# Optimization experiments

Hardware: AMD Instinct MI355X
Metric: run time of the kernel (lower is better)

The kernel has to match this reference:

```python
import jax, jax.numpy as jnp
import numpy as np

B, Q, K, D, H, DH = 4, 512, 4096, 1024, 8, 128  # qk_channels=v_channels=out=1024

def setup_inputs() -> dict:
    key = jax.random.key(0)
    ks = jax.random.split(key, 5)
    s = 1.0 / np.sqrt(D)
    return {
        "inputs_q": jax.random.normal(ks[0], (B, Q, D), jnp.float32),
        "inputs_kv": jax.random.normal(ks[1], (B, K, D), jnp.float32),
        "Wq": jax.random.normal(ks[2], (D, H, DH), jnp.float32) * s,
        "Wkv": jax.random.normal(ks[3], (D, H, 2 * DH), jnp.float32) * s,
        "Wproj": jax.random.normal(ks[4], (H, DH, D), jnp.float32) * (1.0 / np.sqrt(H * DH)),
        "b_proj": jnp.zeros((D,), jnp.float32),
    }

def reference(inputs_q, inputs_kv, Wq, Wkv, Wproj, b_proj):
    # QKV projections (no bias)
    q = jnp.einsum('bqd,dhe->bqhe', inputs_q, Wq)          # [B,Q,H,DH]
    kv = jnp.einsum('bkd,dhe->bkhe', inputs_kv, Wkv)        # [B,K,H,2*DH]
    k, v = kv[..., :DH], kv[..., DH:]
    # scaled dot-product attention (softmax in fp32, per source)
    attn = jnp.einsum('bqhd,bkhd->bhqk', q, k) / np.sqrt(DH)
    attn = jax.nn.softmax(attn.astype(jnp.float32), axis=-1).astype(v.dtype)
    o = jnp.einsum('bhqk,bkhd->bqhd', attn, v)              # [B,Q,H,DH]
    # output projection contracting (head, head_dim), with bias
    return jnp.einsum('bqhd,hdo->bqo', o, Wproj) + b_proj   # [B,Q,D]
```

## Files before the change

### kernel.cpp

```cpp
#include <hip/hip_runtime.h>
#include <hip/hip_bf16.h>
#include <cstdint>

typedef unsigned short u16;
typedef unsigned int u32;
typedef __bf16 bf16x8 __attribute__((ext_vector_type(8)));
typedef u16 u16x8 __attribute__((ext_vector_type(8)));
typedef u16 u16x4 __attribute__((ext_vector_type(4)));
typedef float f32x4 __attribute__((ext_vector_type(4)));

#define MFMA16(a, b, c) __builtin_amdgcn_mfma_f32_16x16x32_bf16(a, b, c, 0, 0, 0)

__device__ __forceinline__ void async16(const void* g, void* s) {
    __builtin_amdgcn_global_load_lds((const __attribute__((address_space(1))) void*)g,
                                     (__attribute__((address_space(3))) void*)s, 16, 0, 0);
}

__device__ __forceinline__ u16 f2bf(float f) {
    u32 u; __builtin_memcpy(&u, &f, 4);
    u = u + 0x7fffu + ((u >> 16) & 1u);
    return (u16)(u >> 16);
}

__global__ __launch_bounds__(256) void convert_inputs(const float* __restrict__ inq,
                                                      u16* __restrict__ Aq,
                                                      const float* __restrict__ inkv,
                                                      u16* __restrict__ Akv) {
    const int blk = blockIdx.x;
    const float* in; u16* out; size_t i;
    if (blk < 1024) { in = inq;  out = Aq;  i = (size_t)blk * 256 + threadIdx.x; }
    else            { in = inkv; out = Akv; i = (size_t)(blk - 1024) * 256 + threadIdx.x; }
    const float4* p = (const float4*)in + i * 2;
    const float4 a = p[0], b = p[1];
    u16x8 v;
    v[0] = f2bf(a.x); v[1] = f2bf(a.y); v[2] = f2bf(a.z); v[3] = f2bf(a.w);
    v[4] = f2bf(b.x); v[5] = f2bf(b.y); v[6] = f2bf(b.z); v[7] = f2bf(b.w);
    ((u16x8*)out)[i] = v;
}

__global__ __launch_bounds__(256) void prep_weights(const float* __restrict__ Wq,  u16* __restrict__ WqT,
                                                    const float* __restrict__ Wkv, u16* __restrict__ WkvT,
                                                    const float* __restrict__ Wp,  u16* __restrict__ WpT) {
    __shared__ u16 t[64][65];
    const int blk = blockIdx.x;
    const float* in; u16* out; int R, C, bx, by;
    if (blk < 256)      { in = Wq;  out = WqT;  R = 1024; C = 1024; bx = blk & 15;  by = blk >> 4; }
    else if (blk < 768) { in = Wkv; out = WkvT; R = 1024; C = 2048; bx = (blk - 256) & 31; by = (blk - 256) >> 5; }
    else                { in = Wp;  out = WpT;  R = 1024; C = 1024; bx = (blk - 768) & 15; by = (blk - 768) >> 4; }
    const int r0 = by << 6, c0 = bx << 6;
    const int tid = threadIdx.x;
#pragma unroll
    for (int i = 0; i < 16; i++) {
        int idx = i * 256 + tid;
        int r = idx >> 6, c = idx & 63;
        t[r][c] = f2bf(in[(size_t)(r0 + r) * C + c0 + c]);
    }
    __syncthreads();
#pragma unroll
    for (int i = 0; i < 16; i++) {
        int idx = i * 256 + tid;
        int c = idx >> 6, r = idx & 63;
        out[(size_t)(c0 + c) * R + r0 + r] = t[r][c];
    }
}

template <bool OUTF32, int NT>
__global__ __launch_bounds__(256) void gemm_bt(const u16* __restrict__ A,
                                               const u16* __restrict__ B,
                                               void* __restrict__ Cv,
                                               const float* __restrict__ bias,
                                               int M, int N, int K) {
    constexpr int NJ = NT / 32;
    __shared__ __align__(16) u16 As[128 * 64];
    __shared__ __align__(16) u16 Bs[NT * 64];
    const int tid = threadIdx.x;
    const int wave = tid >> 6, lane = tid & 63;
    const int lrow = lane & 15, quad = lane >> 4;
    const int nb = N / NT;
    const int bx = blockIdx.x % nb, by = blockIdx.x / nb;
    const long m0 = (long)by << 7, n0 = (long)bx * NT;
    const int wm = (wave >> 1) << 6, wn = (wave & 1) * (NT / 2);

    const f32x4 fz = {0.f, 0.f, 0.f, 0.f};
    f32x4 acc[4][NJ];
#pragma unroll
    for (int i = 0; i < 4; i++)
#pragma unroll
        for (int j = 0; j < NJ; j++) acc[i][j] = fz;

    const int srow = wave * 8 + (lane >> 3);
    const int scol = ((lane & 7) ^ (lane >> 3)) << 3;
    const u16* Ag = A + (m0 + srow) * K + scol;
    const u16* Bg = B + (n0 + srow) * K + scol;
    u16* AsW = &As[wave * 512];
    u16* BsW = &Bs[wave * 512];

    for (int k0 = 0; k0 < K; k0 += 64) {
        __syncthreads();
#pragma unroll
        for (int c = 0; c < 4; c++)
            async16(Ag + (long)c * 32 * K + k0, AsW + c * 2048);
#pragma unroll
        for (int c = 0; c < NT / 32; c++)
            async16(Bg + (long)c * 32 * K + k0, BsW + c * 2048);
        __syncthreads();
#pragma unroll
        for (int c = 0; c < 2; c++) {
            bf16x8 af[4], bfr[NJ];
#pragma unroll
            for (int i = 0; i < 4; i++) {
                const int row = wm + i * 16 + lrow;
                af[i] = *(const bf16x8*)&As[row * 64 + (((c * 4 + quad) ^ (row & 7)) << 3)];
            }
#pragma unroll
            for (int j = 0; j < NJ; j++) {
                const int row = wn + j * 16 + lrow;
                bfr[j] = *(const bf16x8*)&Bs[row * 64 + (((c * 4 + quad) ^ (row & 7)) << 3)];
            }
#pragma unroll
            for (int i = 0; i < 4; i++)
#pragma unroll
                for (int j = 0; j < NJ; j++)
                    acc[i][j] = MFMA16(bfr[j], af[i], acc[i][j]);
        }
    }
#pragma unroll
    for (int i = 0; i < 4; i++) {
        const long row = m0 + wm + i * 16 + lrow;
#pragma unroll
        for (int j = 0; j < NJ; j++) {
            const long colb = n0 + wn + j * 16 + quad * 4;
            if (OUTF32) {
                f32x4 v = acc[i][j];
                if (bias) v += *(const f32x4*)&bias[colb];
                *(f32x4*)&((float*)Cv)[row * N + colb] = v;
            } else {
                u16x4 pk;
#pragma unroll
                for (int r = 0; r < 4; r++) pk[r] = f2bf(acc[i][j][r]);
                *(u16x4*)&((u16*)Cv)[row * N + colb] = pk;
            }
        }
    }
}

__global__ __launch_bounds__(512, 2) void gemm_kv256(const u16* __restrict__ A,
                                                     const u16* __restrict__ B,
                                                     u16* __restrict__ C,
                                                     u16* __restrict__ Vt) {
    constexpr int K = 1024, N = 2048, NT = 16;
    __shared__ __align__(16) u16 As[2][256 * 64];
    __shared__ __align__(16) u16 Bs[2][256 * 64];
    const int tid = threadIdx.x;
    const int wave = tid >> 6, lane = tid & 63;
    const int lrow = lane & 15, quad = lane >> 4;
    const int wMi = wave >> 2, wNi = wave & 3;
    const int wm = wMi * 128, wn = wNi * 64;
    const int wg = blockIdx.x;
    const int swz = (wg & 7) * 64 + (wg >> 3);
    const int bx = swz & 7, by = swz >> 3;
    const long m0 = (long)by << 8, n0 = (long)bx << 8;

    const int srow = tid >> 3;
    const int scol = ((tid & 7) ^ (srow & 7)) << 3;
    const u16* Ag = A + (m0 + srow) * K + scol;
    const u16* Bg = B + (n0 + srow) * K + scol;
    const int sdst = tid * 8;

    auto stgA = [&](int bi, int h, int kt) {
        async16(Ag + (size_t)(h * 128) * K + kt * 64,      &As[bi][h * 8192 + sdst]);
        async16(Ag + (size_t)(h * 128 + 64) * K + kt * 64, &As[bi][h * 8192 + 4096 + sdst]);
    };
    auto stgB = [&](int bi, int h, int kt) {
        async16(Bg + (size_t)(h * 128) * K + kt * 64,      &Bs[bi][h * 8192 + sdst]);
        async16(Bg + (size_t)(h * 128 + 64) * K + kt * 64, &Bs[bi][h * 8192 + 4096 + sdst]);
    };

    stgB(0, 0, 0); stgB(0, 1, 0); stgA(0, 0, 0); stgA(0, 1, 0);
    stgB(1, 0, 1); stgB(1, 1, 1); stgA(1, 0, 1);

    const f32x4 fz = {0.f, 0.f, 0.f, 0.f};
    f32x4 acc[8][4];
#pragma unroll
    for (int i = 0; i < 8; i++)
#pragma unroll
        for (int j = 0; j < 4; j++) acc[i][j] = fz;

    asm volatile("s_waitcnt vmcnt(6)" ::: "memory");
    __builtin_amdgcn_s_barrier();

    bf16x8 av[4][2], bv[4][2];
    for (int t = 0; t < NT; ++t) {
        const int cur = t & 1, nxt = cur ^ 1;
#pragma unroll
        for (int i = 0; i < 4; i++) {
            const int row = wm + i * 16 + lrow;
#pragma unroll
            for (int c = 0; c < 2; c++)
                av[i][c] = *(const bf16x8*)&As[cur][row * 64 + (((c * 4 + quad) ^ (row & 7)) << 3)];
        }
#pragma unroll
        for (int j = 0; j < 4; j++) {
            const int row = wn + j * 16 + lrow;
#pragma unroll
            for (int c = 0; c < 2; c++)
                bv[j][c] = *(const bf16x8*)&Bs[cur][row * 64 + (((c * 4 + quad) ^ (row & 7)) << 3)];
        }
        if (t + 1 < NT) stgA(nxt, 1, t + 1);
        __builtin_amdgcn_s_barrier();
        asm volatile("s_waitcnt lgkmcnt(0)" ::: "memory");
        __builtin_amdgcn_sched_barrier(0);
        __builtin_amdgcn_s_setprio(1);
#pragma unroll
        for (int i = 0; i < 4; i++)
#pragma unroll
            for (int j = 0; j < 2; j++)
#pragma unroll
                for (int c = 0; c < 2; c++)
                    acc[i][j] = MFMA16(av[i][c], bv[j][c], acc[i][j]);
        __builtin_amdgcn_s_setprio(0);
        __builtin_amdgcn_s_barrier();
        if (t + 2 < NT) stgB(cur, 0, t + 2);
        __builtin_amdgcn_s_barrier();
        __builtin_amdgcn_sched_barrier(0);
        __builtin_amdgcn_s_setprio(1);
#pragma unroll
        for (int i = 0; i < 4; i++)
#pragma unroll
            for (int j = 2; j < 4; j++)
#pragma unroll
                for (int c = 0; c < 2; c++)
                    acc[i][j] = MFMA16(av[i][c], bv[j][c], acc[i][j]);
        __builtin_amdgcn_s_setprio(0);
        __builtin_amdgcn_s_barrier();
#pragma unroll
        for (int i = 0; i < 4; i++) {
            const int row = wm + (i + 4) * 16 + lrow;
#pragma unroll
            for (int c = 0; c < 2; c++)
                av[i][c] = *(const bf16x8*)&As[cur][row * 64 + (((c * 4 + quad) ^ (row & 7)) << 3)];
        }
        if (t + 2 < NT) stgB(cur, 1, t + 2);
        __builtin_amdgcn_s_barrier();
        asm volatile("s_waitcnt lgkmcnt(0)" ::: "memory");
        __builtin_amdgcn_sched_barrier(0);
        __builtin_amdgcn_s_setprio(1);
#pragma unroll
        for (int i = 0; i < 4; i++)
#pragma unroll
            for (int j = 0; j < 2; j++)
#pragma unroll
                for (int c = 0; c < 2; c++)
                    acc[i + 4][j] = MFMA16(av[i][c], bv[j][c], acc[i + 4][j]);
        __builtin_amdgcn_s_setprio(0);
        __builtin_amdgcn_s_barrier();
        if (t + 2 < NT) stgA(cur, 0, t + 2);
        __builtin_amdgcn_s_barrier();
        __builtin_amdgcn_sched_barrier(0);
        __builtin_amdgcn_s_setprio(1);
#pragma unroll
        for (int i = 0; i < 4; i++)
#pragma unroll
            for (int j = 2; j < 4; j++)
#pragma unroll
                for (int c = 0; c < 2; c++)
                    acc[i + 4][j] = MFMA16(av[i][c], bv[j][c], acc[i + 4][j]);
        __builtin_amdgcn_s_setprio(0);
        if (t + 2 < NT)      { asm volatile("s_waitcnt vmcnt(6)" ::: "memory"); }
        else if (t + 1 < NT) { asm volatile("s_waitcnt vmcnt(0)" ::: "memory"); }
        __builtin_amdgcn_s_barrier();
    }

    const int h = bx;
    if (wNi < 2) {
#pragma unroll
        for (int j = 0; j < 4; j++) {
            const long col = n0 + wn + j * 16 + lrow;
#pragma unroll
            for (int i = 0; i < 8; i++) {
                const long row = m0 + wm + i * 16 + quad * 4;
#pragma unroll
                for (int r = 0; r < 4; r++)
                    C[(row + r) * N + col] = f2bf(acc[i][j][r]);
            }
        }
    } else {
#pragma unroll
        for (int j = 0; j < 4; j++) {
            const int dh = (wNi - 2) * 64 + j * 16 + lrow;
#pragma unroll
            for (int i = 0; i < 8; i++) {
                const int row = (int)m0 + wm + i * 16 + quad * 4;
                const int b = row >> 12, kv = row & 4095;
                u16x4 pk;
#pragma unroll
                for (int r = 0; r < 4; r++) pk[r] = f2bf(acc[i][j][r]);
                *(u16x4*)&Vt[(((size_t)b * 8 + h) * 128 + dh) * 4096 + kv] = pk;
            }
        }
    }
}

__global__ __launch_bounds__(512, 4) void flash_attn_split(const u16* __restrict__ qb,
                                                           const u16* __restrict__ kvb,
                                                           const u16* __restrict__ vTb,
                                                           float* __restrict__ Opart,
                                                           float* __restrict__ Mpart,
                                                           float* __restrict__ Lpart) {
    __shared__ __align__(16) u16 Ks[2][64 * 128];
    __shared__ __align__(16) u16 Vs[2][128 * 64];
    __shared__ __align__(16) u16 Ps[8][16 * 64];
    const int tid = threadIdx.x, wave = tid >> 6, lane = tid & 63;
    const int lrow = lane & 15, quad = lane >> 4;
    const int blk = blockIdx.x;
    const int split = blk & 3, qt = (blk >> 2) & 3, h = (blk >> 4) & 7, b = blk >> 7;
    const int q0 = qt * 128;
    const int kbase = split * 1024;

    bf16x8 qf[4];
    {
        const u16* qp = qb + (((size_t)(b * 512 + q0 + wave * 16 + lrow) * 8 + h) << 7) + quad * 8;
#pragma unroll
        for (int c = 0; c < 4; c++) qf[c] = *(const bf16x8*)(qp + c * 32);
    }

    const f32x4 fz = {0.f, 0.f, 0.f, 0.f};
    f32x4 oacc[8];
#pragma unroll
    for (int g = 0; g < 8; g++) oacc[g] = fz;
    float mrow = -1e30f, lsum = 0.f;
    const float scale = 0.08838834764831845f;

    const int kRow = tid >> 4, kBlk = tid & 15;
    const int vRow = tid >> 3, vBlk = tid & 7;
    const u16* kg = kvb + (size_t)b * 4096 * 2048 + h * 256 + kBlk * 8;
    const u16* vg = vTb + (size_t)(b * 8 + h) * 128 * 4096 + vBlk * 8;
    const int ksw = (kBlk ^ (kRow & 15)) << 3;
    const int vsw = (vBlk ^ (vRow & 7)) << 3;

    {
        const bf16x8 a0 = *(const bf16x8*)&kg[(size_t)(kbase + kRow) * 2048];
        const bf16x8 a1 = *(const bf16x8*)&kg[(size_t)(kbase + 32 + kRow) * 2048];
        const bf16x8 b0 = *(const bf16x8*)&vg[(size_t)vRow * 4096 + kbase];
        const bf16x8 b1 = *(const bf16x8*)&vg[(size_t)(64 + vRow) * 4096 + kbase];
        *(bf16x8*)&Ks[0][kRow * 128 + ksw] = a0;
        *(bf16x8*)&Ks[0][(32 + kRow) * 128 + ksw] = a1;
        *(bf16x8*)&Vs[0][vRow * 64 + vsw] = b0;
        *(bf16x8*)&Vs[0][(64 + vRow) * 64 + vsw] = b1;
    }
    __syncthreads();

    for (int it = 0; it < 16; ++it) {
        const int cur = it & 1, nxt = cur ^ 1;
        const bool more = (it + 1 < 16);
        bf16x8 nk0, nk1, nv0, nv1;
        if (more) {
            const int k1 = kbase + (it + 1) * 64;
            nk0 = *(const bf16x8*)&kg[(size_t)(k1 + kRow) * 2048];
            nk1 = *(const bf16x8*)&kg[(size_t)(k1 + 32 + kRow) * 2048];
            nv0 = *(const bf16x8*)&vg[(size_t)vRow * 4096 + k1];
            nv1 = *(const bf16x8*)&vg[(size_t)(64 + vRow) * 4096 + k1];
        }

        f32x4 s[4];
        __builtin_amdgcn_s_setprio(1);
#pragma unroll
        for (int t = 0; t < 4; t++) {
            f32x4 a = fz;
#pragma unroll
            for (int c = 0; c < 4; c++) {
                const bf16x8 kf = *(const bf16x8*)
                    &Ks[cur][(t * 16 + lrow) * 128 + (((c * 4 + quad) ^ lrow) << 3)];
                a = MFMA16(kf, qf[c], a);
            }
            s[t] = a * scale;
        }
        __builtin_amdgcn_s_setprio(0);

        float mx = s[0][0];
#pragma unroll
        for (int t = 0; t < 4; t++)
#pragma unroll
            for (int r = 0; r < 4; r++) mx = fmaxf(mx, s[t][r]);
        mx = fmaxf(mx, __shfl_xor(mx, 16));
        mx = fmaxf(mx, __shfl_xor(mx, 32));
        float mn = fmaxf(mrow, mx);
        if (__all(mx <= mrow + 8.f)) {
            mn = mrow;
        } else {
            const float alpha = __expf(mrow - mn);
#pragma unroll
            for (int g = 0; g < 8; g++) oacc[g] *= alpha;
            lsum *= alpha;
            mrow = mn;
        }
        float sum = 0.f;
#pragma unroll
        for (int t = 0; t < 4; t++)
#pragma unroll
            for (int r = 0; r < 4; r++) {
                float p = __expf(s[t][r] - mn);
                s[t][r] = p;
                sum += p;
            }
        sum += __shfl_xor(sum, 16);
        sum += __shfl_xor(sum, 32);
        lsum += sum;

        u16* Pw = &Ps[wave][0];
#pragma unroll
        for (int t = 0; t < 4; t++) {
            u16x4 pk;
#pragma unroll
            for (int r = 0; r < 4; r++) pk[r] = f2bf(s[t][r]);
            const int kvo = t * 16 + quad * 4;
            *(u16x4*)&Pw[lrow * 64 + (((kvo >> 3) ^ (lrow & 7)) << 3) + (kvo & 7)] = pk;
        }
        asm volatile("s_waitcnt lgkmcnt(0)" ::: "memory");
        __builtin_amdgcn_sched_barrier(0);
        const bf16x8 pf0 = *(const bf16x8*)&Pw[lrow * 64 + ((quad ^ (lrow & 7)) << 3)];
        const bf16x8 pf1 = *(const bf16x8*)&Pw[lrow * 64 + (((4 + quad) ^ (lrow & 7)) << 3)];

        __builtin_amdgcn_s_setprio(1);
#pragma unroll
        for (int g = 0; g < 8; g++) {
            f32x4 o = oacc[g];
            o = MFMA16(*(const bf16x8*)&Vs[cur][(g * 16 + lrow) * 64 + ((quad ^ (lrow & 7)) << 3)], pf0, o);
            o = MFMA16(*(const bf16x8*)&Vs[cur][(g * 16 + lrow) * 64 + (((4 + quad) ^ (lrow & 7)) << 3)], pf1, o);
            oacc[g] = o;
        }
        __builtin_amdgcn_s_setprio(0);

        if (more) {
            *(bf16x8*)&Ks[nxt][kRow * 128 + ksw] = nk0;
            *(bf16x8*)&Ks[nxt][(32 + kRow) * 128 + ksw] = nk1;
            *(bf16x8*)&Vs[nxt][vRow * 64 + vsw] = nv0;
            *(bf16x8*)&Vs[nxt][(64 + vRow) * 64 + vsw] = nv1;
        }
        __syncthreads();
    }

    float* Ob = Opart + (size_t)blk * 16384;
#pragma unroll
    for (int g = 0; g < 8; g++)
        *(f32x4*)&Ob[(wave * 16 + lrow) * 128 + g * 16 + quad * 4] = oacc[g];
    if (quad == 0) {
        const int row = blk * 128 + wave * 16 + lrow;
        Mpart[row] = mrow;
        Lpart[row] = lsum;
    }
}

__global__ __launch_bounds__(512) void combine_attn(const float* __restrict__ Opart,
                                                    const float* __restrict__ Mpart,
                                                    const float* __restrict__ Lpart,
                                                    u16* __restrict__ ob) {
    const int c = blockIdx.x;
    const int qt = c & 3, h = (c >> 2) & 7, b = c >> 5;
    const int lr = threadIdx.x >> 2, cg = (threadIdx.x & 3) * 32;
    float ms[4], w[4];
    float m = -1e30f;
#pragma unroll
    for (int s = 0; s < 4; s++) { ms[s] = Mpart[(c * 4 + s) * 128 + lr]; m = fmaxf(m, ms[s]); }
    float l = 0.f;
#pragma unroll
    for (int s = 0; s < 4; s++) { w[s] = __expf(ms[s] - m); l += w[s] * Lpart[(c * 4 + s) * 128 + lr]; }
    const float inv = 1.f / l;
#pragma unroll
    for (int s = 0; s < 4; s++) w[s] *= inv;
    const size_t orow = ((size_t)(b * 512 + qt * 128 + lr) * 8 + h) << 7;
#pragma unroll
    for (int j = 0; j < 4; j++) {
        f32x4 a0 = {0.f, 0.f, 0.f, 0.f}, a1 = a0;
#pragma unroll
        for (int s = 0; s < 4; s++) {
            const f32x4* p = (const f32x4*)(Opart + ((size_t)(c * 4 + s)) * 16384 + (size_t)lr * 128 + cg + j * 8);
            a0 += p[0] * w[s];
            a1 += p[1] * w[s];
        }
        u16x8 v;
#pragma unroll
        for (int i = 0; i < 4; i++) { v[i] = f2bf(a0[i]); v[4 + i] = f2bf(a1[i]); }
        *(u16x8*)&ob[orow + cg + j * 8] = v;
    }
}

extern "C" void kernel_launch(void* const* d_in, const int* in_sizes, int n_in,
                              void* d_out, int out_size, void* d_ws, size_t ws_size,
                              hipStream_t stream) {
    const float* inq   = (const float*)d_in[0];
    const float* inkv  = (const float*)d_in[1];
    const float* Wq    = (const float*)d_in[2];
    const float* Wkv   = (const float*)d_in[3];
    const float* Wproj = (const float*)d_in[4];
    const float* bproj = (const float*)d_in[5];
    float* out = (float*)d_out;

    u16* WqT    = (u16*)d_ws;
    u16* WkvT   = WqT + (size_t)1024 * 1024;
    u16* WprojT = WkvT + (size_t)2048 * 1024;
    u16* Aq     = WprojT + (size_t)1024 * 1024;
    u16* Akv    = Aq + (size_t)2048 * 1024;
    u16* qbuf   = Akv + (size_t)16384 * 1024;
    u16* kvbuf  = qbuf + (size_t)2048 * 1024;
    u16* vTbuf  = kvbuf + (size_t)16384 * 2048;
    u16* obuf   = vTbuf + (size_t)32 * 128 * 4096;

    float* Opart = (float*)Akv;
    float* Mpart = (float*)Aq;
    float* Lpart = Mpart + 65536;

    convert_inputs<<<9216, 256, 0, stream>>>(inq, Aq, inkv, Akv);
    prep_weights<<<1024, 256, 0, stream>>>(Wq, WqT, Wkv, WkvT, Wproj, WprojT);

    gemm_bt<false, 64><<<16 * 16, 256, 0, stream>>>(Aq, WqT, qbuf, nullptr, 2048, 1024, 1024);
    gemm_kv256<<<512, 512, 0, stream>>>(Akv, WkvT, kvbuf, vTbuf);

    flash_attn_split<<<512, 512, 0, stream>>>(qbuf, kvbuf, vTbuf, Opart, Mpart, Lpart);
    combine_attn<<<128, 512, 0, stream>>>(Opart, Mpart, Lpart, obuf);

    gemm_bt<true, 64><<<16 * 16, 256, 0, stream>>>(obuf, WprojT, (void*)out, bproj, 2048, 1024, 1024);
}
```

Measured before the change: 303.9 us.

## Process 32 query rows per wave in flash attention to reuse K/V tiles

Each wave now handles two 16-row query fragments, so every block covers 256 query rows and each K/V tile loaded into LDS feeds twice as many MFMAs. The grid halves to 256 blocks, block indices are remapped for locality, and the combine kernel is resized to match. The intent is to cut K/V global and LDS traffic per unit of compute, at the cost of more registers (occupancy bound lowered to 2) and fewer blocks, which is about one per CU on MI355X.

```diff
diff --git a/kernel.cpp b/kernel.cpp
--- a/kernel.cpp
+++ b/kernel.cpp
@@ -301,7 +301,7 @@
     }
 }
 
-__global__ __launch_bounds__(512, 4) void flash_attn_split(const u16* __restrict__ qb,
+__global__ __launch_bounds__(512, 2) void flash_attn_split(const u16* __restrict__ qb,
                                                            const u16* __restrict__ kvb,
                                                            const u16* __restrict__ vTb,
                                                            float* __restrict__ Opart,
@@ -309,26 +309,30 @@
                                                            float* __restrict__ Lpart) {
     __shared__ __align__(16) u16 Ks[2][64 * 128];
     __shared__ __align__(16) u16 Vs[2][128 * 64];
-    __shared__ __align__(16) u16 Ps[8][16 * 64];
+    __shared__ __align__(16) u16 Ps[8][32 * 64];
     const int tid = threadIdx.x, wave = tid >> 6, lane = tid & 63;
     const int lrow = lane & 15, quad = lane >> 4;
-    const int blk = blockIdx.x;
-    const int split = blk & 3, qt = (blk >> 2) & 3, h = (blk >> 4) & 7, b = blk >> 7;
-    const int q0 = qt * 128;
+    const int p = blockIdx.x;
+    const int lg = (p & 7) * 32 + (p >> 3);
+    const int split = lg & 3, qt = (lg >> 2) & 1, h = (lg >> 3) & 7, b = lg >> 6;
+    const int q0 = qt * 256;
     const int kbase = split * 1024;
 
-    bf16x8 qf[4];
-    {
-        const u16* qp = qb + (((size_t)(b * 512 + q0 + wave * 16 + lrow) * 8 + h) << 7) + quad * 8;
-#pragma unroll
-        for (int c = 0; c < 4; c++) qf[c] = *(const bf16x8*)(qp + c * 32);
+    bf16x8 qf[2][4];
+#pragma unroll
+    for (int rf = 0; rf < 2; rf++) {
+        const u16* qp = qb + (((size_t)(b * 512 + q0 + wave * 32 + rf * 16 + lrow) * 8 + h) << 7) + quad * 8;
+#pragma unroll
+        for (int c = 0; c < 4; c++) qf[rf][c] = *(const bf16x8*)(qp + c * 32);
     }
 
     const f32x4 fz = {0.f, 0.f, 0.f, 0.f};
-    f32x4 oacc[8];
-#pragma unroll
-    for (int g = 0; g < 8; g++) oacc[g] = fz;
-    float mrow = -1e30f, lsum = 0.f;
+    f32x4 oacc[2][8];
+#pragma unroll
+    for (int rf = 0; rf < 2; rf++)
+#pragma unroll
+        for (int g = 0; g < 8; g++) oacc[rf][g] = fz;
+    float mrow[2] = {-1e30f, -1e30f}, lsum[2] = {0.f, 0.f};
     const float scale = 0.08838834764831845f;
 
     const int kRow = tid >> 4, kBlk = tid & 15;
@@ -362,72 +366,91 @@
             nv1 = *(const bf16x8*)&vg[(size_t)(64 + vRow) * 4096 + k1];
         }
 
-        f32x4 s[4];
+        f32x4 s[2][4];
         __builtin_amdgcn_s_setprio(1);
 #pragma unroll
         for (int t = 0; t < 4; t++) {
-            f32x4 a = fz;
+            f32x4 a0 = fz, a1 = fz;
 #pragma unroll
             for (int c = 0; c < 4; c++) {
                 const bf16x8 kf = *(const bf16x8*)
                     &Ks[cur][(t * 16 + lrow) * 128 + (((c * 4 + quad) ^ lrow) << 3)];
-                a = MFMA16(kf, qf[c], a);
-            }
-            s[t] = a * scale;
+                a0 = MFMA16(kf, qf[0][c], a0);
+                a1 = MFMA16(kf, qf[1][c], a1);
+            }
+            s[0][t] = a0 * scale;
+            s[1][t] = a1 * scale;
         }
         __builtin_amdgcn_s_setprio(0);
 
-        float mx = s[0][0];
-#pragma unroll
-        for (int t = 0; t < 4; t++)
-#pragma unroll
-            for (int r = 0; r < 4; r++) mx = fmaxf(mx, s[t][r]);
-        mx = fmaxf(mx, __shfl_xor(mx, 16));
-        mx = fmaxf(mx, __shfl_xor(mx, 32));
-        float mn = fmaxf(mrow, mx);
-        if (__all(mx <= mrow + 8.f)) {
-            mn = mrow;
-        } else {
-            const float alpha = __expf(mrow - mn);
-#pragma unroll
-            for (int g = 0; g < 8; g++) oacc[g] *= alpha;
-            lsum *= alpha;
-            mrow = mn;
-        }
-        float sum = 0.f;
-#pragma unroll
-        for (int t = 0; t < 4; t++)
-#pragma unroll
-            for (int r = 0; r < 4; r++) {
-                float p = __expf(s[t][r] - mn);
-                s[t][r] = p;
-                sum += p;
-            }
-        sum += __shfl_xor(sum, 16);
-        sum += __shfl_xor(sum, 32);
-        lsum += sum;
+#pragma unroll
+        for (int rf = 0; rf < 2; rf++) {
+            float mx = s[rf][0][0];
+#pragma unroll
+            for (int t = 0; t < 4; t++)
+#pragma unroll
+                for (int r = 0; r < 4; r++) mx = fmaxf(mx, s[rf][t][r]);
+            mx = fmaxf(mx, __shfl_xor(mx, 16));
+            mx = fmaxf(mx, __shfl_xor(mx, 32));
+            float mn = fmaxf(mrow[rf], mx);
+            if (__all(mx <= mrow[rf] + 8.f)) {
+                mn = mrow[rf];
+            } else {
+                const float alpha = __expf(mrow[rf] - mn);
+#pragma unroll
+                for (int g = 0; g < 8; g++) oacc[rf][g] *= alpha;
+                lsum[rf] *= alpha;
+                mrow[rf] = mn;
+            }
+            float sum = 0.f;
+#pragma unroll
+            for (int t = 0; t < 4; t++)
+#pragma unroll
+                for (int r = 0; r < 4; r++) {
+                    float pv = __expf(s[rf][t][r] - mn);
+                    s[rf][t][r] = pv;
+                    sum += pv;
+                }
+            sum += __shfl_xor(sum, 16);
+            sum += __shfl_xor(sum, 32);
+            lsum[rf] += sum;
+        }
 
         u16* Pw = &Ps[wave][0];
 #pragma unroll
-        for (int t = 0; t < 4; t++) {
-            u16x4 pk;
-#pragma unroll
-            for (int r = 0; r < 4; r++) pk[r] = f2bf(s[t][r]);
-            const int kvo = t * 16 + quad * 4;
-            *(u16x4*)&Pw[lrow * 64 + (((kvo >> 3) ^ (lrow & 7)) << 3) + (kvo & 7)] = pk;
+        for (int rf = 0; rf < 2; rf++) {
+            const int prow = rf * 16 + lrow;
+#pragma unroll
+            for (int t = 0; t < 4; t++) {
+                u16x4 pk;
+#pragma unroll
+                for (int r = 0; r < 4; r++) pk[r] = f2bf(s[rf][t][r]);
+                const int kvo = t * 16 + quad * 4;
+                *(u16x4*)&Pw[prow * 64 + (((kvo >> 3) ^ (prow & 7)) << 3) + (kvo & 7)] = pk;
+            }
         }
         asm volatile("s_waitcnt lgkmcnt(0)" ::: "memory");
         __builtin_amdgcn_sched_barrier(0);
-        const bf16x8 pf0 = *(const bf16x8*)&Pw[lrow * 64 + ((quad ^ (lrow & 7)) << 3)];
-        const bf16x8 pf1 = *(const bf16x8*)&Pw[lrow * 64 + (((4 + quad) ^ (lrow & 7)) << 3)];
+        bf16x8 pf[2][2];
+#pragma unroll
+        for (int rf = 0; rf < 2; rf++) {
+            const int prow = rf * 16 + lrow;
+            pf[rf][0] = *(const bf16x8*)&Pw[prow * 64 + ((quad ^ (prow & 7)) << 3)];
+            pf[rf][1] = *(const bf16x8*)&Pw[prow * 64 + (((4 + quad) ^ (prow & 7)) << 3)];
+        }
 
         __builtin_amdgcn_s_setprio(1);
 #pragma unroll
         for (int g = 0; g < 8; g++) {
-            f32x4 o = oacc[g];
-            o = MFMA16(*(const bf16x8*)&Vs[cur][(g * 16 + lrow) * 64 + ((quad ^ (lrow & 7)) << 3)], pf0, o);
-            o = MFMA16(*(const bf16x8*)&Vs[cur][(g * 16 + lrow) * 64 + (((4 + quad) ^ (lrow & 7)) << 3)], pf1, o);
-            oacc[g] = o;
+            const bf16x8 v0 = *(const bf16x8*)&Vs[cur][(g * 16 + lrow) * 64 + ((quad ^ (lrow & 7)) << 3)];
+            const bf16x8 v1 = *(const bf16x8*)&Vs[cur][(g * 16 + lrow) * 64 + (((4 + quad) ^ (lrow & 7)) << 3)];
+#pragma unroll
+            for (int rf = 0; rf < 2; rf++) {
+                f32x4 o = oacc[rf][g];
+                o = MFMA16(v0, pf[rf][0], o);
+                o = MFMA16(v1, pf[rf][1], o);
+                oacc[rf][g] = o;
+            }
         }
         __builtin_amdgcn_s_setprio(0);
 
@@ -440,14 +463,19 @@
         __syncthreads();
     }
 
-    float* Ob = Opart + (size_t)blk * 16384;
-#pragma unroll
-    for (int g = 0; g < 8; g++)
-        *(f32x4*)&Ob[(wave * 16 + lrow) * 128 + g * 16 + quad * 4] = oacc[g];
+    float* Ob = Opart + (size_t)lg * 32768;
+#pragma unroll
+    for (int rf = 0; rf < 2; rf++)
+#pragma unroll
+        for (int g = 0; g < 8; g++)
+            *(f32x4*)&Ob[(wave * 32 + rf * 16 + lrow) * 128 + g * 16 + quad * 4] = oacc[rf][g];
     if (quad == 0) {
-        const int row = blk * 128 + wave * 16 + lrow;
-        Mpart[row] = mrow;
-        Lpart[row] = lsum;
+#pragma unroll
+        for (int rf = 0; rf < 2; rf++) {
+            const int row = lg * 256 + wave * 32 + rf * 16 + lrow;
+            Mpart[row] = mrow[rf];
+            Lpart[row] = lsum[rf];
+        }
     }
 }
 
@@ -455,28 +483,28 @@
                                                     const float* __restrict__ Mpart,
                                                     const float* __restrict__ Lpart,
                                                     u16* __restrict__ ob) {
-    const int c = blockIdx.x;
-    const int qt = c & 3, h = (c >> 2) & 7, b = c >> 5;
-    const int lr = threadIdx.x >> 2, cg = (threadIdx.x & 3) * 32;
+    const int g = blockIdx.x;
+    const int qt = g & 1, h = (g >> 1) & 7, b = g >> 4;
+    const int lr = threadIdx.x >> 1, cg = (threadIdx.x & 1) * 64;
     float ms[4], w[4];
     float m = -1e30f;
 #pragma unroll
-    for (int s = 0; s < 4; s++) { ms[s] = Mpart[(c * 4 + s) * 128 + lr]; m = fmaxf(m, ms[s]); }
+    for (int s = 0; s < 4; s++) { ms[s] = Mpart[(g * 4 + s) * 256 + lr]; m = fmaxf(m, ms[s]); }
     float l = 0.f;
 #pragma unroll
-    for (int s = 0; s < 4; s++) { w[s] = __expf(ms[s] - m); l += w[s] * Lpart[(c * 4 + s) * 128 + lr]; }
+    for (int s = 0; s < 4; s++) { w[s] = __expf(ms[s] - m); l += w[s] * Lpart[(g * 4 + s) * 256 + lr]; }
     const float inv = 1.f / l;
 #pragma unroll
     for (int s = 0; s < 4; s++) w[s] *= inv;
-    const size_t orow = ((size_t)(b * 512 + qt * 128 + lr) * 8 + h) << 7;
-#pragma unroll
-    for (int j = 0; j < 4; j++) {
+    const size_t orow = ((size_t)(b * 512 + qt * 256 + lr) * 8 + h) << 7;
+#pragma unroll
+    for (int j = 0; j < 8; j++) {
         f32x4 a0 = {0.f, 0.f, 0.f, 0.f}, a1 = a0;
 #pragma unroll
         for (int s = 0; s < 4; s++) {
-            const f32x4* p = (const f32x4*)(Opart + ((size_t)(c * 4 + s)) * 16384 + (size_t)lr * 128 + cg + j * 8);
-            a0 += p[0] * w[s];
-            a1 += p[1] * w[s];
+            const f32x4* pp = (const f32x4*)(Opart + ((size_t)(g * 4 + s)) * 32768 + (size_t)lr * 128 + cg + j * 8);
+            a0 += pp[0] * w[s];
+            a1 += pp[1] * w[s];
         }
         u16x8 v;
 #pragma unroll
@@ -516,8 +544,8 @@
     gemm_bt<false, 64><<<16 * 16, 256, 0, stream>>>(Aq, WqT, qbuf, nullptr, 2048, 1024, 1024);
     gemm_kv256<<<512, 512, 0, stream>>>(Akv, WkvT, kvbuf, vTbuf);
 
-    flash_attn_split<<<512, 512, 0, stream>>>(qbuf, kvbuf, vTbuf, Opart, Mpart, Lpart);
-    combine_attn<<<128, 512, 0, stream>>>(Opart, Mpart, Lpart, obuf);
+    flash_attn_split<<<256, 512, 0, stream>>>(qbuf, kvbuf, vTbuf, Opart, Mpart, Lpart);
+    combine_attn<<<64, 512, 0, stream>>>(Opart, Mpart, Lpart, obuf);
 
     gemm_bt<true, 64><<<16 * 16, 256, 0, stream>>>(obuf, WprojT, (void*)out, bproj, 2048, 1024, 1024);
 }
```

Result: slower. 313.3 us (+3.1%).

## Rewrite flash attention with 32x32 MFMA, register-resident P, async LDS loads

Applied to the files above, without the earlier changes.

The flash attention kernel moves from 16x16x32 to 32x32x16 bf16 MFMA, with 4 waves each owning 32 query rows. The P tile now stays in registers, packed with v_cvt_pk_bf16 and v_permlane32_swap instead of a round trip through LDS. K/V staging uses direct global-to-LDS async loads, and softmax switches to exp2 with a prescaled log2e factor. The KV split drops from 4 to 2 (256 blocks with XCD-aware remapping), and the combine kernel is reduced to two partials. This is meant to cut LDS traffic, instruction count and combine work, at the cost of fewer blocks and less parallelism across the GPU.

```diff
diff --git a/kernel.cpp b/kernel.cpp
--- a/kernel.cpp
+++ b/kernel.cpp
@@ -8,8 +8,11 @@
 typedef u16 u16x8 __attribute__((ext_vector_type(8)));
 typedef u16 u16x4 __attribute__((ext_vector_type(4)));
 typedef float f32x4 __attribute__((ext_vector_type(4)));
+typedef float f32x16 __attribute__((ext_vector_type(16)));
+typedef u32 u32x4 __attribute__((ext_vector_type(4)));
 
 #define MFMA16(a, b, c) __builtin_amdgcn_mfma_f32_16x16x32_bf16(a, b, c, 0, 0, 0)
+#define MFMA32(a, b, c) __builtin_amdgcn_mfma_f32_32x32x16_bf16(a, b, c, 0, 0, 0)
 
 __device__ __forceinline__ void async16(const void* g, void* s) {
     __builtin_amdgcn_global_load_lds((const __attribute__((address_space(1))) void*)g,
@@ -20,6 +23,15 @@
     u32 u; __builtin_memcpy(&u, &f, 4);
     u = u + 0x7fffu + ((u >> 16) & 1u);
     return (u16)(u >> 16);
+}
+
+__device__ __forceinline__ u32 cvtpk(float lo, float hi) {
+    u32 r;
+    asm("v_cvt_pk_bf16_f32 %0, %1, %2" : "=v"(r) : "v"(lo), "v"(hi));
+    return r;
+}
+__device__ __forceinline__ void plswap(u32& a, u32& b) {
+    asm volatile("v_permlane32_swap_b32 %0, %1" : "+v"(a), "+v"(b));
 }
 
 __global__ __launch_bounds__(256) void convert_inputs(const float* __restrict__ inq,
@@ -301,7 +313,7 @@
     }
 }
 
-__global__ __launch_bounds__(512, 4) void flash_attn_split(const u16* __restrict__ qb,
+__global__ __launch_bounds__(256, 2) void flash_attn_split(const u16* __restrict__ qb,
                                                            const u16* __restrict__ kvb,
                                                            const u16* __restrict__ vTb,
                                                            float* __restrict__ Opart,
@@ -309,143 +321,146 @@
                                                            float* __restrict__ Lpart) {
     __shared__ __align__(16) u16 Ks[2][64 * 128];
     __shared__ __align__(16) u16 Vs[2][128 * 64];
-    __shared__ __align__(16) u16 Ps[8][16 * 64];
     const int tid = threadIdx.x, wave = tid >> 6, lane = tid & 63;
-    const int lrow = lane & 15, quad = lane >> 4;
-    const int blk = blockIdx.x;
-    const int split = blk & 3, qt = (blk >> 2) & 3, h = (blk >> 4) & 7, b = blk >> 7;
-    const int q0 = qt * 128;
-    const int kbase = split * 1024;
-
-    bf16x8 qf[4];
+    const int lq = lane & 31, hi = lane >> 5;
+    const int p = blockIdx.x;
+    const int lg = (p & 7) * 32 + (p >> 3);
+    const int split = lg & 1, qblk = (lg >> 1) & 3, h = (lg >> 3) & 7, b = lg >> 6;
+    const int kbase = split * 2048;
+
+    bf16x8 qf[8];
     {
-        const u16* qp = qb + (((size_t)(b * 512 + q0 + wave * 16 + lrow) * 8 + h) << 7) + quad * 8;
-#pragma unroll
-        for (int c = 0; c < 4; c++) qf[c] = *(const bf16x8*)(qp + c * 32);
-    }
-
-    const f32x4 fz = {0.f, 0.f, 0.f, 0.f};
-    f32x4 oacc[8];
-#pragma unroll
-    for (int g = 0; g < 8; g++) oacc[g] = fz;
+        const u16* qp = qb + (((size_t)(b * 512 + qblk * 128 + wave * 32 + lq) * 8 + h) << 7) + hi * 8;
+#pragma unroll
+        for (int ks = 0; ks < 8; ks++) qf[ks] = *(const bf16x8*)(qp + ks * 16);
+    }
+
+    f32x16 oacc[4];
+#pragma unroll
+    for (int dt = 0; dt < 4; dt++)
+#pragma unroll
+        for (int r = 0; r < 16; r++) oacc[dt][r] = 0.f;
     float mrow = -1e30f, lsum = 0.f;
-    const float scale = 0.08838834764831845f;
-
-    const int kRow = tid >> 4, kBlk = tid & 15;
-    const int vRow = tid >> 3, vBlk = tid & 7;
-    const u16* kg = kvb + (size_t)b * 4096 * 2048 + h * 256 + kBlk * 8;
-    const u16* vg = vTb + (size_t)(b * 8 + h) * 128 * 4096 + vBlk * 8;
-    const int ksw = (kBlk ^ (kRow & 15)) << 3;
-    const int vsw = (vBlk ^ (vRow & 7)) << 3;
-
-    {
-        const bf16x8 a0 = *(const bf16x8*)&kg[(size_t)(kbase + kRow) * 2048];
-        const bf16x8 a1 = *(const bf16x8*)&kg[(size_t)(kbase + 32 + kRow) * 2048];
-        const bf16x8 b0 = *(const bf16x8*)&vg[(size_t)vRow * 4096 + kbase];
-        const bf16x8 b1 = *(const bf16x8*)&vg[(size_t)(64 + vRow) * 4096 + kbase];
-        *(bf16x8*)&Ks[0][kRow * 128 + ksw] = a0;
-        *(bf16x8*)&Ks[0][(32 + kRow) * 128 + ksw] = a1;
-        *(bf16x8*)&Vs[0][vRow * 64 + vsw] = b0;
-        *(bf16x8*)&Vs[0][(64 + vRow) * 64 + vsw] = b1;
-    }
+    const float scale2 = 0.08838834764831845f * 1.4426950408889634f;
+    const float THR2 = 11.5415603f;
+
+    const int kR = tid >> 4, kC = tid & 15, kS = kC ^ (kR & 15);
+    const int vR = tid >> 3, vC = tid & 7,  vS = vC ^ (vR & 7);
+    const u16* kgp = kvb + (size_t)b * 4096 * 2048 + h * 256 + kS * 8;
+    const u16* vgp = vTb + (size_t)(b * 8 + h) * 128 * 4096 + vS * 8;
+
+    auto stage = [&](int bi, int k0) {
+#pragma unroll
+        for (int pp = 0; pp < 4; pp++)
+            async16(kgp + (size_t)(k0 + pp * 16 + kR) * 2048, &Ks[bi][pp * 2048 + tid * 8]);
+#pragma unroll
+        for (int pp = 0; pp < 4; pp++)
+            async16(vgp + (size_t)(pp * 32 + vR) * 4096 + k0, &Vs[bi][pp * 2048 + tid * 8]);
+    };
+
+    stage(0, kbase);
+    asm volatile("s_waitcnt vmcnt(0)" ::: "memory");
     __syncthreads();
 
-    for (int it = 0; it < 16; ++it) {
+    for (int it = 0; it < 32; ++it) {
         const int cur = it & 1, nxt = cur ^ 1;
-        const bool more = (it + 1 < 16);
-        bf16x8 nk0, nk1, nv0, nv1;
-        if (more) {
-            const int k1 = kbase + (it + 1) * 64;
-            nk0 = *(const bf16x8*)&kg[(size_t)(k1 + kRow) * 2048];
-            nk1 = *(const bf16x8*)&kg[(size_t)(k1 + 32 + kRow) * 2048];
-            nv0 = *(const bf16x8*)&vg[(size_t)vRow * 4096 + k1];
-            nv1 = *(const bf16x8*)&vg[(size_t)(64 + vRow) * 4096 + k1];
-        }
-
-        f32x4 s[4];
+        if (it + 1 < 32) stage(nxt, kbase + (it + 1) * 64);
+
+        f32x16 s[2];
         __builtin_amdgcn_s_setprio(1);
 #pragma unroll
-        for (int t = 0; t < 4; t++) {
-            f32x4 a = fz;
-#pragma unroll
-            for (int c = 0; c < 4; c++) {
-                const bf16x8 kf = *(const bf16x8*)
-                    &Ks[cur][(t * 16 + lrow) * 128 + (((c * 4 + quad) ^ lrow) << 3)];
-                a = MFMA16(kf, qf[c], a);
-            }
-            s[t] = a * scale;
+        for (int t = 0; t < 2; t++) {
+            f32x16 a;
+#pragma unroll
+            for (int r = 0; r < 16; r++) a[r] = 0.f;
+#pragma unroll
+            for (int ks = 0; ks < 8; ks++) {
+                const int row = t * 32 + lq;
+                const int c = ks * 2 + hi;
+                const bf16x8 kf = *(const bf16x8*)&Ks[cur][row * 128 + ((c ^ (row & 15)) << 3)];
+                a = MFMA32(kf, qf[ks], a);
+            }
+#pragma unroll
+            for (int r = 0; r < 16; r++) s[t][r] = a[r] * scale2;
         }
         __builtin_amdgcn_s_setprio(0);
 
         float mx = s[0][0];
 #pragma unroll
-        for (int t = 0; t < 4; t++)
-#pragma unroll
-            for (int r = 0; r < 4; r++) mx = fmaxf(mx, s[t][r]);
-        mx = fmaxf(mx, __shfl_xor(mx, 16));
+        for (int t = 0; t < 2; t++)
+#pragma unroll
+            for (int r = 0; r < 16; r++) mx = fmaxf(mx, s[t][r]);
         mx = fmaxf(mx, __shfl_xor(mx, 32));
         float mn = fmaxf(mrow, mx);
-        if (__all(mx <= mrow + 8.f)) {
+        if (__all(mx <= mrow + THR2)) {
             mn = mrow;
         } else {
-            const float alpha = __expf(mrow - mn);
-#pragma unroll
-            for (int g = 0; g < 8; g++) oacc[g] *= alpha;
+            const float alpha = exp2f(mrow - mn);
+#pragma unroll
+            for (int dt = 0; dt < 4; dt++)
+#pragma unroll
+                for (int r = 0; r < 16; r++) oacc[dt][r] *= alpha;
             lsum *= alpha;
             mrow = mn;
         }
         float sum = 0.f;
 #pragma unroll
-        for (int t = 0; t < 4; t++)
-#pragma unroll
-            for (int r = 0; r < 4; r++) {
-                float p = __expf(s[t][r] - mn);
-                s[t][r] = p;
-                sum += p;
-            }
-        sum += __shfl_xor(sum, 16);
+        for (int t = 0; t < 2; t++)
+#pragma unroll
+            for (int r = 0; r < 16; r++) {
+                const float pv = exp2f(s[t][r] - mn);
+                s[t][r] = pv;
+                sum += pv;
+            }
         sum += __shfl_xor(sum, 32);
         lsum += sum;
 
-        u16* Pw = &Ps[wave][0];
-#pragma unroll
-        for (int t = 0; t < 4; t++) {
-            u16x4 pk;
-#pragma unroll
-            for (int r = 0; r < 4; r++) pk[r] = f2bf(s[t][r]);
-            const int kvo = t * 16 + quad * 4;
-            *(u16x4*)&Pw[lrow * 64 + (((kvo >> 3) ^ (lrow & 7)) << 3) + (kvo & 7)] = pk;
-        }
-        asm volatile("s_waitcnt lgkmcnt(0)" ::: "memory");
-        __builtin_amdgcn_sched_barrier(0);
-        const bf16x8 pf0 = *(const bf16x8*)&Pw[lrow * 64 + ((quad ^ (lrow & 7)) << 3)];
-        const bf16x8 pf1 = *(const bf16x8*)&Pw[lrow * 64 + (((4 + quad) ^ (lrow & 7)) << 3)];
+        bf16x8 pb[4];
+#pragma unroll
+        for (int sl = 0; sl < 4; sl++) {
+            const int t = sl >> 1, k8 = (sl & 1) * 8;
+            u32 d1 = cvtpk(s[t][k8 + 0], s[t][k8 + 1]);
+            u32 d2 = cvtpk(s[t][k8 + 2], s[t][k8 + 3]);
+            u32 s1 = cvtpk(s[t][k8 + 4], s[t][k8 + 5]);
+            u32 s2 = cvtpk(s[t][k8 + 6], s[t][k8 + 7]);
+            plswap(d1, s1);
+            plswap(d2, s2);
+            u32x4 w; w[0] = d1; w[1] = d2; w[2] = s1; w[3] = s2;
+            __builtin_memcpy(&pb[sl], &w, 16);
+        }
 
         __builtin_amdgcn_s_setprio(1);
 #pragma unroll
-        for (int g = 0; g < 8; g++) {
-            f32x4 o = oacc[g];
-            o = MFMA16(*(const bf16x8*)&Vs[cur][(g * 16 + lrow) * 64 + ((quad ^ (lrow & 7)) << 3)], pf0, o);
-            o = MFMA16(*(const bf16x8*)&Vs[cur][(g * 16 + lrow) * 64 + (((4 + quad) ^ (lrow & 7)) << 3)], pf1, o);
-            oacc[g] = o;
+        for (int dt = 0; dt < 4; dt++) {
+            f32x16 o = oacc[dt];
+#pragma unroll
+            for (int sl = 0; sl < 4; sl++) {
+                const int row = dt * 32 + lq;
+                const int c = sl * 2 + hi;
+                const bf16x8 vf = *(const bf16x8*)&Vs[cur][row * 64 + ((c ^ (row & 7)) << 3)];
+                o = MFMA32(vf, pb[sl], o);
+            }
+            oacc[dt] = o;
         }
         __builtin_amdgcn_s_setprio(0);
 
-        if (more) {
-            *(bf16x8*)&Ks[nxt][kRow * 128 + ksw] = nk0;
-            *(bf16x8*)&Ks[nxt][(32 + kRow) * 128 + ksw] = nk1;
-            *(bf16x8*)&Vs[nxt][vRow * 64 + vsw] = nv0;
-            *(bf16x8*)&Vs[nxt][(64 + vRow) * 64 + vsw] = nv1;
-        }
+        asm volatile("s_waitcnt vmcnt(0)" ::: "memory");
         __syncthreads();
     }
 
-    float* Ob = Opart + (size_t)blk * 16384;
-#pragma unroll
-    for (int g = 0; g < 8; g++)
-        *(f32x4*)&Ob[(wave * 16 + lrow) * 128 + g * 16 + quad * 4] = oacc[g];
-    if (quad == 0) {
-        const int row = blk * 128 + wave * 16 + lrow;
+    float* Ob = Opart + (size_t)lg * 16384;
+    const int qrow = wave * 32 + lq;
+#pragma unroll
+    for (int dt = 0; dt < 4; dt++)
+#pragma unroll
+        for (int g = 0; g < 4; g++) {
+            f32x4 v;
+#pragma unroll
+            for (int r = 0; r < 4; r++) v[r] = oacc[dt][g * 4 + r];
+            *(f32x4*)&Ob[qrow * 128 + dt * 32 + g * 8 + hi * 4] = v;
+        }
+    if (hi == 0) {
+        const int row = lg * 128 + qrow;
         Mpart[row] = mrow;
         Lpart[row] = lsum;
     }
@@ -455,29 +470,23 @@
                                                     const float* __restrict__ Mpart,
                                                     const float* __restrict__ Lpart,
                                                     u16* __restrict__ ob) {
-    const int c = blockIdx.x;
-    const int qt = c & 3, h = (c >> 2) & 7, b = c >> 5;
+    const int g = blockIdx.x;
+    const int qblk = g & 3, h = (g >> 2) & 7, b = g >> 5;
     const int lr = threadIdx.x >> 2, cg = (threadIdx.x & 3) * 32;
-    float ms[4], w[4];
-    float m = -1e30f;
-#pragma unroll
-    for (int s = 0; s < 4; s++) { ms[s] = Mpart[(c * 4 + s) * 128 + lr]; m = fmaxf(m, ms[s]); }
-    float l = 0.f;
-#pragma unroll
-    for (int s = 0; s < 4; s++) { w[s] = __expf(ms[s] - m); l += w[s] * Lpart[(c * 4 + s) * 128 + lr]; }
+    const int lg0 = g * 2, lg1 = g * 2 + 1;
+    const float m0 = Mpart[lg0 * 128 + lr], m1 = Mpart[lg1 * 128 + lr];
+    const float m = fmaxf(m0, m1);
+    float w0 = exp2f(m0 - m), w1 = exp2f(m1 - m);
+    const float l = w0 * Lpart[lg0 * 128 + lr] + w1 * Lpart[lg1 * 128 + lr];
     const float inv = 1.f / l;
-#pragma unroll
-    for (int s = 0; s < 4; s++) w[s] *= inv;
-    const size_t orow = ((size_t)(b * 512 + qt * 128 + lr) * 8 + h) << 7;
+    w0 *= inv; w1 *= inv;
+    const size_t orow = ((size_t)(b * 512 + qblk * 128 + lr) * 8 + h) << 7;
+    const float* p0 = Opart + (size_t)lg0 * 16384 + (size_t)lr * 128 + cg;
+    const float* p1 = Opart + (size_t)lg1 * 16384 + (size_t)lr * 128 + cg;
 #pragma unroll
     for (int j = 0; j < 4; j++) {
-        f32x4 a0 = {0.f, 0.f, 0.f, 0.f}, a1 = a0;
-#pragma unroll
-        for (int s = 0; s < 4; s++) {
-            const f32x4* p = (const f32x4*)(Opart + ((size_t)(c * 4 + s)) * 16384 + (size_t)lr * 128 + cg + j * 8);
-            a0 += p[0] * w[s];
-            a1 += p[1] * w[s];
-        }
+        const f32x4 a0 = ((const f32x4*)p0)[j * 2]     * w0 + ((const f32x4*)p1)[j * 2]     * w1;
+        const f32x4 a1 = ((const f32x4*)p0)[j * 2 + 1] * w0 + ((const f32x4*)p1)[j * 2 + 1] * w1;
         u16x8 v;
 #pragma unroll
         for (int i = 0; i < 4; i++) { v[i] = f2bf(a0[i]); v[4 + i] = f2bf(a1[i]); }
@@ -516,7 +525,7 @@
     gemm_bt<false, 64><<<16 * 16, 256, 0, stream>>>(Aq, WqT, qbuf, nullptr, 2048, 1024, 1024);
     gemm_kv256<<<512, 512, 0, stream>>>(Akv, WkvT, kvbuf, vTbuf);
 
-    flash_attn_split<<<512, 512, 0, stream>>>(qbuf, kvbuf, vTbuf, Opart, Mpart, Lpart);
+    flash_attn_split<<<256, 256, 0, stream>>>(qbuf, kvbuf, vTbuf, Opart, Mpart, Lpart);
     combine_attn<<<128, 512, 0, stream>>>(Opart, Mpart, Lpart, obuf);
 
     gemm_bt<true, 64><<<16 * 16, 256, 0, stream>>>(obuf, WprojT, (void*)out, bproj, 2048, 1024, 1024);
```

Measured after the change: 319.6 us. 5.2% more time.
